# Kernel optimization log

Hardware: AMD Instinct MI355X
Metric: run time of the kernel (lower is better)

The kernel has to match this reference:

```python
import jax, jax.numpy as jnp
import numpy as np
import math

B, S, D, H, HD, R, F = 2, 2048, 1024, 16, 64, 32, 4096
EPS = 1e-5

def _layernorm(x, g, b):
    mu = jnp.mean(x, axis=-1, keepdims=True)
    var = jnp.mean(jnp.square(x - mu), axis=-1, keepdims=True)
    return (x - mu) * jax.lax.rsqrt(var + EPS) * g + b

def _gelu(x):
    # faithful tanh-approximation from the module
    c = math.sqrt(2.0 / math.pi)
    return 0.5 * x * (1.0 + jnp.tanh(c * (x + 0.044715 * x ** 3)))

def setup_inputs() -> dict:
    key = jax.random.key(0)
    ks = jax.random.split(key, 8)
    s = 0.02
    return dict(
        x=jax.random.normal(ks[0], (B, S, D), jnp.float32),
        ln1_g=jnp.ones((D,), jnp.float32), ln1_b=jnp.zeros((D,), jnp.float32),
        Wq=jax.random.normal(ks[1], (H, D, HD), jnp.float32) * s,
        bq=jnp.zeros((H, HD), jnp.float32),
        Wk=jax.random.normal(ks[2], (H, D, HD), jnp.float32) * s,
        bk=jnp.zeros((H, HD), jnp.float32),
        Wvd=jax.random.normal(ks[3], (H, D, R), jnp.float32) * s,
        bvd=jnp.zeros((H, R), jnp.float32),
        Wvu=jax.random.normal(ks[4], (H, R, HD), jnp.float32) * s,
        bvu=jnp.zeros((H, HD), jnp.float32),
        ln2_g=jnp.ones((D,), jnp.float32), ln2_b=jnp.zeros((D,), jnp.float32),
        W1=jax.random.normal(ks[5], (D, F), jnp.float32) * s,
        b1=jnp.zeros((F,), jnp.float32),
        W2=jax.random.normal(ks[6], (F, D), jnp.float32) * s,
        b2=jnp.zeros((D,), jnp.float32),
    )

def reference(x, ln1_g, ln1_b, Wq, bq, Wk, bk, Wvd, bvd, Wvu, bvu,
              ln2_g, ln2_b, W1, b1, W2, b2):
    Bx, Sx, Dx = x.shape
    y = x
    h = _layernorm(x, ln1_g, ln1_b)
    # all heads batched: [B,H,S,HD]
    q = jnp.einsum('bsd,hde->bhse', h, Wq) + bq[None, :, None, :]
    k = jnp.einsum('bsd,hde->bhse', h, Wk) + bk[None, :, None, :]
    vd = jnp.einsum('bsd,hdr->bhsr', h, Wvd) + bvd[None, :, None, :]
    v = jnp.einsum('bhsr,hre->bhse', vd, Wvu) + bvu[None, :, None, :]
    scores = jnp.einsum('bhse,bhte->bhst', q, k) / math.sqrt(Dx)  # NB: scaled by embed dim, as in source
    i = jnp.arange(Sx)
    mask = i[None, :] < i[:, None]  # key index < query index is masked (reversed causal, faithful)
    scores = jnp.where(mask[None, None, :, :], -jnp.inf, scores)
    attn = jax.nn.softmax(scores, axis=-1)
    o = jnp.einsum('bhst,bhte->bhse', attn, v)
    o = o.transpose(0, 2, 1, 3).reshape(Bx, Sx, Dx)  # concat heads
    x = o + y
    y = x
    h = _layernorm(x, ln2_g, ln2_b)
    h = _gelu(h @ W1 + b1)
    h = h @ W2 + b2
    return h + y
```

## Files before the change

kernel.cpp:

```cpp
#include <hip/hip_runtime.h>


typedef unsigned short u16;
typedef __attribute__((ext_vector_type(4))) float f32x4;
typedef __attribute__((ext_vector_type(8))) __bf16 bf16x8;

#define B_ 2
#define S_ 2048
#define D_ 1024
#define H_ 16
#define HD_ 64
#define R_ 32
#define F_ 4096
#define M_ (B_ * S_)
#define NQKV 2560
#define C2F 0.04508422002778011f

__device__ __forceinline__ u16 f2bf(float f) {
  union { float f; unsigned u; } v; v.f = f;
  unsigned u = v.u;
  return (u16)((u + 0x7FFFu + ((u >> 16) & 1u)) >> 16);
}
__device__ __forceinline__ float bf2f(u16 h) {
  union { unsigned u; float f; } v; v.u = ((unsigned)h) << 16;
  return v.f;
}
__device__ __forceinline__ unsigned pk_bf16(float lo, float hi) {
  unsigned r;
  asm volatile("v_cvt_pk_bf16_f32 %0, %1, %2" : "=v"(r) : "v"(lo), "v"(hi));
  return r;
}

typedef __attribute__((address_space(1))) void gvoid;
typedef __attribute__((address_space(3))) void lvoid;
__device__ __forceinline__ void gload_lds16(const void* g, void* l) {
  __builtin_amdgcn_global_load_lds((gvoid*)(void*)g, (lvoid*)l, 16, 0, 0);
}

__device__ __forceinline__ float gelu_f(float x) {
  float t = tanhf(0.7978845608028654f * (x + 0.044715f * x * x * x));
  return 0.5f * x * (1.0f + t);
}

__global__ __launch_bounds__(256) void wtrans(const float* __restrict__ in,
                                              u16* __restrict__ out,
                                              int Rr, int Cc, long ibs, long obs,
                                              float scale) {
  __shared__ float tile[32][33];
  const float* ip = in + (size_t)blockIdx.z * ibs;
  u16* op = out + (size_t)blockIdx.z * obs;
  int c0 = blockIdx.x * 32, r0 = blockIdx.y * 32;
  int tx = threadIdx.x & 31, ty = threadIdx.x >> 5;
#pragma unroll
  for (int j = 0; j < 32; j += 8)
    tile[ty + j][tx] = ip[(size_t)(r0 + ty + j) * Cc + c0 + tx];
  __syncthreads();
#pragma unroll
  for (int j = 0; j < 32; j += 8)
    op[(size_t)(c0 + ty + j) * Rr + r0 + tx] = f2bf(tile[tx][ty + j] * scale);
}

__global__ __launch_bounds__(256) void wconv(const float* __restrict__ in,
                                             u16* __restrict__ out, int n) {
  int i = (blockIdx.x * 256 + threadIdx.x) * 4;
  if (i < n) {
    float4 v = *(const float4*)&in[i];
    ushort4 o;
    o.x = f2bf(v.x); o.y = f2bf(v.y); o.z = f2bf(v.z); o.w = f2bf(v.w);
    *(ushort4*)&out[i] = o;
  }
}

__global__ __launch_bounds__(256) void bconcat(const float* __restrict__ bq,
                                               const float* __restrict__ bk,
                                               const float* __restrict__ bvd,
                                               float* __restrict__ o) {
  int i = blockIdx.x * 256 + threadIdx.x;
  if (i < NQKV) {
    float v = (i < 1024) ? bq[i] * C2F : (i < 2048 ? bk[i - 1024] : bvd[i - 2048]);
    o[i] = v;
  }
}

__global__ __launch_bounds__(256) void ln_kernel(const float* __restrict__ xin,
                                                 const float* __restrict__ addin,
                                                 const float* __restrict__ gam,
                                                 const float* __restrict__ bet,
                                                 u16* __restrict__ hout,
                                                 float* __restrict__ x2out) {
  int row = blockIdx.x, tid = threadIdx.x;
  size_t base = (size_t)row * D_ + tid * 4;
  float4 v = *(const float4*)&xin[base];
  if (addin) {
    float4 a = *(const float4*)&addin[base];
    v.x += a.x; v.y += a.y; v.z += a.z; v.w += a.w;
  }
  if (x2out) *(float4*)&x2out[base] = v;
  float s = v.x + v.y + v.z + v.w;
  float ss = v.x * v.x + v.y * v.y + v.z * v.z + v.w * v.w;
#pragma unroll
  for (int off = 32; off > 0; off >>= 1) {
    s += __shfl_down(s, off);
    ss += __shfl_down(ss, off);
  }
  __shared__ float red[8];
  int wv = tid >> 6;
  if ((tid & 63) == 0) { red[wv] = s; red[4 + wv] = ss; }
  __syncthreads();
  if (tid == 0) {
    float s1 = red[0] + red[1] + red[2] + red[3];
    float s2 = red[4] + red[5] + red[6] + red[7];
    float mu = s1 * (1.0f / D_);
    red[0] = mu;
    red[1] = s2 * (1.0f / D_) - mu * mu;
  }
  __syncthreads();
  float mu = red[0];
  float rstd = rsqrtf(red[1] + 1e-5f);
  int ci = tid * 4;
  ushort4 o;
  o.x = f2bf((v.x - mu) * rstd * gam[ci + 0] + bet[ci + 0]);
  o.y = f2bf((v.y - mu) * rstd * gam[ci + 1] + bet[ci + 1]);
  o.z = f2bf((v.z - mu) * rstd * gam[ci + 2] + bet[ci + 2]);
  o.w = f2bf((v.w - mu) * rstd * gam[ci + 3] + bet[ci + 3]);
  *(ushort4*)&hout[base] = o;
}

template <int MODE>
__global__ __launch_bounds__(256) void gemm_nt(const u16* __restrict__ A,
                                               const u16* __restrict__ Bt,
                                               int K, int lda, int ldb,
                                               const float* __restrict__ bias,
                                               const float* __restrict__ res,
                                               void* __restrict__ Cout,
                                               void* __restrict__ Cout2, int ldc) {
  __shared__ __align__(16) u16 As0[128 * 32];
  __shared__ __align__(16) u16 Bs0[128 * 32];
  __shared__ __align__(16) u16 As1[128 * 32];
  __shared__ __align__(16) u16 Bs1[128 * 32];
  int tid = threadIdx.x;
  int lane = tid & 63, wid = tid >> 6;
  int wm = wid >> 1, wn = wid & 1;
  int row0 = blockIdx.y * 128, col0 = blockIdx.x * 128;
  int l15 = lane & 15, g = lane >> 4;
  int srow = lane >> 2, scol = (lane & 3) * 8;
  f32x4 acc[4][4] = {};
  const u16* Ap = A + (size_t)row0 * lda;
  const u16* Bp = Bt + (size_t)col0 * ldb;

  auto STAGE = [&](u16* AS, u16* BS, int kk) {
#pragma unroll
    for (int i = 0; i < 2; ++i) {
      int c = wid * 2 + i;
      gload_lds16(Ap + (size_t)(c * 16 + srow) * lda + kk + scol, &AS[c * 512]);
      gload_lds16(Bp + (size_t)(c * 16 + srow) * ldb + kk + scol, &BS[c * 512]);
    }
  };
  auto COMPUTE = [&](const u16* AS, const u16* BS) {
    bf16x8 af[4], bfr[4];
#pragma unroll
    for (int t = 0; t < 4; ++t) {
      af[t] = *(const bf16x8*)&AS[(wm * 64 + t * 16 + l15) * 32 + g * 8];
      bfr[t] = *(const bf16x8*)&BS[(wn * 64 + t * 16 + l15) * 32 + g * 8];
    }
#pragma unroll
    for (int mt = 0; mt < 4; ++mt)
#pragma unroll
      for (int nt = 0; nt < 4; ++nt)
        acc[mt][nt] = __builtin_amdgcn_mfma_f32_16x16x32_bf16(af[mt], bfr[nt],
                                                              acc[mt][nt], 0, 0, 0);
  };

  STAGE(As0, Bs0, 0);
  __syncthreads();
  for (int k0 = 0; k0 < K; k0 += 64) {
    if (k0 + 32 < K) STAGE(As1, Bs1, k0 + 32);
    COMPUTE(As0, Bs0);
    __syncthreads();
    if (k0 + 64 < K) STAGE(As0, Bs0, k0 + 64);
    COMPUTE(As1, Bs1);
    __syncthreads();
  }

#pragma unroll
  for (int mt = 0; mt < 4; ++mt) {
#pragma unroll
    for (int nt = 0; nt < 4; ++nt) {
      int cc = col0 + wn * 64 + nt * 16 + l15;
      float bv = bias ? bias[cc] : 0.0f;
#pragma unroll
      for (int j = 0; j < 4; ++j) {
        int rr = row0 + wm * 64 + mt * 16 + g * 4 + j;
        float v = acc[mt][nt][j] + bv;
        if (MODE == 1) v = gelu_f(v);
        if (MODE == 2) {
          ((float*)Cout)[(size_t)rr * ldc + cc] = v + res[(size_t)rr * ldc + cc];
        } else {
          ((u16*)Cout)[(size_t)rr * ldc + cc] = f2bf(v);
        }
      }
    }
  }
  (void)Cout2;
}

template <int MODE>
__global__ __launch_bounds__(512, 2) void gemm8(
    const u16* __restrict__ A, const u16* __restrict__ Bt,
    int lda, int ldb, int nk,
    const float* __restrict__ bias,
    float* __restrict__ Cf, u16* __restrict__ Cb,
    u16* __restrict__ P1, u16* __restrict__ P2, u16* __restrict__ P3,
    int ldc) {
  extern __shared__ __align__(16) char smem[];
  int tid = threadIdx.x;
  int lane = tid & 63, wid = tid >> 6;
  int wm = wid >> 2, wn = wid & 3;
  int l15 = lane & 15, g = lane >> 4;
  int row0 = blockIdx.y * 256, col0 = blockIdx.x * 256;
  int koff = blockIdx.z * (nk * 64);
  const u16* Ap = A + (size_t)row0 * lda + koff;
  const u16* Bp = Bt + (size_t)col0 * ldb + koff;
  int trow = tid >> 3;
  int sbyte = ((tid & 7) * 16) ^ ((trow & 7) << 4);
  int xr = (l15 & 7) << 4;

  f32x4 acc[8][4] = {};

  auto STAGE_A = [&](int buf, int kt) {
#pragma unroll
    for (int l = 0; l < 4; ++l)
      gload_lds16((const char*)(Ap + (size_t)(l * 64 + trow) * lda + kt) + sbyte,
                  smem + buf * 65536 + (l * 64 + wid * 8) * 128);
  };
  auto STAGE_B = [&](int buf, int kt) {
#pragma unroll
    for (int l = 0; l < 4; ++l)
      gload_lds16((const char*)(Bp + (size_t)(l * 64 + trow) * ldb + kt) + sbyte,
                  smem + buf * 65536 + 32768 + (l * 64 + wid * 8) * 128);
  };

  STAGE_A(0, 0);
  STAGE_B(0, 0);
  asm volatile("s_waitcnt vmcnt(0)" ::: "memory");
  __builtin_amdgcn_sched_barrier(0);
  __builtin_amdgcn_s_barrier();

  int cur = 0;
  for (int it = 0; it < nk; ++it) {
    const char* Ab = smem + cur * 65536 + (wm * 128 + l15) * 128;
    const char* Bb = smem + cur * 65536 + 32768 + (wn * 64 + l15) * 128;
    bool nxt = (it + 1 < nk);
#pragma unroll
    for (int kk = 0; kk < 2; ++kk) {
      int kq = (kk * 64 + g * 16) ^ xr;
      bf16x8 bfr[4], af[8];
#pragma unroll
      for (int nt = 0; nt < 4; ++nt)
        bfr[nt] = *(const bf16x8*)(Bb + nt * 2048 + kq);
#pragma unroll
      for (int mt = 0; mt < 8; ++mt)
        af[mt] = *(const bf16x8*)(Ab + mt * 2048 + kq);
      if (nxt) {
        if (kk == 0) STAGE_A(cur ^ 1, (it + 1) * 64);
        else         STAGE_B(cur ^ 1, (it + 1) * 64);
      }
      __builtin_amdgcn_s_setprio(1);
#pragma unroll
      for (int mt = 0; mt < 8; ++mt)
#pragma unroll
        for (int nt = 0; nt < 4; ++nt)
          acc[mt][nt] = __builtin_amdgcn_mfma_f32_16x16x32_bf16(af[mt], bfr[nt],
                                                                acc[mt][nt], 0, 0, 0);
      __builtin_amdgcn_s_setprio(0);
    }
    asm volatile("s_waitcnt vmcnt(0)" ::: "memory");
    __builtin_amdgcn_sched_barrier(0);
    __builtin_amdgcn_s_barrier();
    cur ^= 1;
  }

  u16* pp = (u16*)nullptr;
  if (MODE == 4 && blockIdx.z != 0)
    pp = (blockIdx.z == 1) ? P1 : (blockIdx.z == 2 ? P2 : P3);
#pragma unroll
  for (int mt = 0; mt < 8; ++mt) {
#pragma unroll
    for (int nt = 0; nt < 4; ++nt) {
      int cc = col0 + wn * 64 + nt * 16 + l15;
      float bv = (MODE == 1) ? bias[cc] : 0.0f;
#pragma unroll
      for (int j = 0; j < 4; ++j) {
        int rr = row0 + wm * 128 + mt * 16 + g * 4 + j;
        float v = acc[mt][nt][j] + bv;
        if (MODE == 1) {
          Cb[(size_t)rr * ldc + cc] = f2bf(gelu_f(v));
        } else {
          if (blockIdx.z == 0) Cf[(size_t)rr * ldc + cc] = v;
          else                 pp[(size_t)rr * ldc + cc] = f2bf(v);
        }
      }
    }
  }
}

__global__ __launch_bounds__(256) void reduce2(float* __restrict__ out,
                                               const u16* __restrict__ p1,
                                               const u16* __restrict__ p2,
                                               const u16* __restrict__ p3,
                                               const float* __restrict__ b2,
                                               const float* __restrict__ x2) {
  int i = (blockIdx.x * 256 + threadIdx.x) * 4;
  float4 o = *(float4*)&out[i];
  ushort4 a = *(const ushort4*)&p1[i];
  ushort4 b = *(const ushort4*)&p2[i];
  ushort4 c = *(const ushort4*)&p3[i];
  float4 r = *(const float4*)&x2[i];
  int cix = i & (D_ - 1);
  o.x += bf2f(a.x) + bf2f(b.x) + bf2f(c.x) + b2[cix + 0] + r.x;
  o.y += bf2f(a.y) + bf2f(b.y) + bf2f(c.y) + b2[cix + 1] + r.y;
  o.z += bf2f(a.z) + bf2f(b.z) + bf2f(c.z) + b2[cix + 2] + r.z;
  o.w += bf2f(a.w) + bf2f(b.w) + bf2f(c.w) + b2[cix + 3] + r.w;
  *(float4*)&out[i] = o;
}

__global__ __launch_bounds__(256) void vu_kernel(const u16* __restrict__ vd,
                                                 const u16* __restrict__ wvu,
                                                 const float* __restrict__ bvu,
                                                 u16* __restrict__ v_t) {
  int t0 = blockIdx.x * 64, h = blockIdx.y, b = blockIdx.z;
  __shared__ u16 vds[64][32];
  __shared__ u16 vt[64][65];
  int tid = threadIdx.x;
  {
    int rr2 = tid >> 2, c8 = (tid & 3) * 8;
    *(bf16x8*)&vds[rr2][c8] =
        *(const bf16x8*)&vd[(size_t)(b * S_ + t0 + rr2) * NQKV + 2048 + h * R_ + c8];
  }
  __syncthreads();
  int e = tid & 63, tg = (tid >> 6) * 16;
  float wcol[32];
#pragma unroll
  for (int r = 0; r < 32; ++r) wcol[r] = bf2f(wvu[((size_t)h * R_ + r) * HD_ + e]);
  float bb = bvu[h * HD_ + e];
  for (int i = 0; i < 16; ++i) {
    int t = tg + i;
    float acc = bb;
#pragma unroll
    for (int r = 0; r < 32; ++r) acc += bf2f(vds[t][r]) * wcol[r];
    vt[t][e] = f2bf(acc);
  }
  __syncthreads();
  for (int idx = tid; idx < 64 * 64; idx += 256) {
    int e2 = idx >> 6, t2 = idx & 63;
    v_t[((size_t)(b * H_ + h) * HD_ + e2) * S_ + t0 + t2] = vt[t2][e2];
  }
}

__global__ __launch_bounds__(512, 2) void attn_kernel(const u16* __restrict__ cqkv,
                                                      const u16* __restrict__ v_t,
                                                      float* __restrict__ o) {
  extern __shared__ __align__(16) u16 kv[];
  __shared__ u16 Pl[8][16 * 64];
  int tid = threadIdx.x;
  int lane = tid & 63, w = tid >> 6;
  int h = blockIdx.x, b = blockIdx.y;
  int bx = blockIdx.z;
  int r = lane & 15, g = lane >> 4;
  const u16* qp = cqkv + (size_t)(b * S_) * NQKV + h * HD_;
  const u16* kp = cqkv + (size_t)(b * S_) * NQKV + 1024 + h * HD_;
  const u16* vp = v_t + (size_t)(b * H_ + h) * HD_ * S_;
  u16* Pw = Pl[w];

  int srow = w * 8 + (lane >> 3);
  int ssw = ((lane & 7) * 16) ^ (((lane >> 3) & 7) << 4);

  int xr = (r & 7) << 4;
  int kq0 = ((g * 16) ^ xr) >> 1;
  int kq1 = ((64 + g * 16) ^ xr) >> 1;

  auto STAGE = [&](int buf, int kt) {
    u16* base = kv + buf * 8192;
    gload_lds16((const char*)(kp + (size_t)(kt + srow) * NQKV) + ssw,
                base + w * 512);
    gload_lds16((const char*)(vp + (size_t)srow * S_ + kt) + ssw,
                base + 4096 + w * 512);
  };

#pragma unroll 1
  for (int half = 0; half < 2; ++half) {
    int qb = half ? (S_ - 128) - bx * 128 : bx * 128;
    int s0 = qb + w * 16;
    int qrow = s0 + r;

    gload_lds16((const char*)(qp + (size_t)(s0 + (lane >> 3)) * NQKV) + ssw, Pw);
    gload_lds16((const char*)(qp + (size_t)(s0 + 8 + (lane >> 3)) * NQKV) + ssw,
                Pw + 512);
    asm volatile("s_waitcnt vmcnt(0)" ::: "memory");
    __builtin_amdgcn_sched_barrier(0);
    __builtin_amdgcn_s_barrier();
    __builtin_amdgcn_sched_barrier(0);
    bf16x8 aq0 = *(const bf16x8*)&Pw[(r << 6) + kq0];
    bf16x8 aq1 = *(const bf16x8*)&Pw[(r << 6) + kq1];

    f32x4 oa[4] = {};
    float m_ = -1e30f, l_ = 0.0f;

    int nt = (S_ - qb) >> 6;
    STAGE(0, qb);
    STAGE(1, qb + 64);

    for (int it = 0; it < nt; ++it) {
      int kt = qb + it * 64;
      if (it + 1 < nt) {
        asm volatile("s_waitcnt vmcnt(2)" ::: "memory");
      } else {
        asm volatile("s_waitcnt vmcnt(0)" ::: "memory");
      }
      __builtin_amdgcn_sched_barrier(0);
      __builtin_amdgcn_s_barrier();
      __builtin_amdgcn_sched_barrier(0);
      if (it + 2 < nt) STAGE((it + 2) % 3, qb + (it + 2) * 64);

      if (kt + 64 > s0) {
        const u16* Kb = kv + (it % 3) * 8192;
        const u16* Vb = Kb + 4096;

        f32x4 sc[4] = {};
#pragma unroll
        for (int blk = 0; blk < 4; ++blk) {
          bf16x8 a0 = *(const bf16x8*)&Kb[((blk * 16 + r) << 6) + kq0];
          bf16x8 a1 = *(const bf16x8*)&Kb[((blk * 16 + r) << 6) + kq1];
          sc[blk] = __builtin_amdgcn_mfma_f32_16x16x32_bf16(a0, aq0, sc[blk], 0, 0, 0);
          sc[blk] = __builtin_amdgcn_mfma_f32_16x16x32_bf16(a1, aq1, sc[blk], 0, 0, 0);
        }

        float p[16];
        if ((qrow & ~63) == kt) {
#pragma unroll
          for (int blk = 0; blk < 4; ++blk)
#pragma unroll
            for (int j = 0; j < 4; ++j) {
              int kk = kt + blk * 16 + g * 4 + j;
              p[blk * 4 + j] = (kk < qrow) ? -1e30f : sc[blk][j];
            }
        } else {
#pragma unroll
          for (int blk = 0; blk < 4; ++blk)
#pragma unroll
            for (int j = 0; j < 4; ++j) p[blk * 4 + j] = sc[blk][j];
        }
        float mx = p[0];
#pragma unroll
        for (int i = 1; i < 16; ++i) mx = fmaxf(mx, p[i]);
        mx = fmaxf(mx, __shfl_xor(mx, 16));
        mx = fmaxf(mx, __shfl_xor(mx, 32));
        float mn = fmaxf(m_, mx);
        float scl = __builtin_amdgcn_exp2f(m_ - mn);
        m_ = mn;
        float sm = 0.0f;
#pragma unroll
        for (int i = 0; i < 16; ++i) {
          p[i] = __builtin_amdgcn_exp2f(p[i] - mn);
          sm += p[i];
        }
        sm += __shfl_xor(sm, 16);
        sm += __shfl_xor(sm, 32);
        l_ = l_ * scl + sm;
#pragma unroll
        for (int et = 0; et < 4; ++et) oa[et] *= scl;

#pragma unroll
        for (int blk = 0; blk < 4; ++blk) {
          uint2 pk;
          pk.x = pk_bf16(p[blk * 4 + 0], p[blk * 4 + 1]);
          pk.y = pk_bf16(p[blk * 4 + 2], p[blk * 4 + 3]);
          *(uint2*)&Pw[(r << 6) + ((((blk << 5) + (g << 3)) ^ xr) >> 1)] = pk;
        }
        asm volatile("s_waitcnt lgkmcnt(0)" ::: "memory");
        __builtin_amdgcn_sched_barrier(0);
        bf16x8 pb0 = *(const bf16x8*)&Pw[(r << 6) + kq0];
        bf16x8 pb1 = *(const bf16x8*)&Pw[(r << 6) + kq1];
#pragma unroll
        for (int et = 0; et < 4; ++et) {
          bf16x8 v0 = *(const bf16x8*)&Vb[((et * 16 + r) << 6) + kq0];
          bf16x8 v1 = *(const bf16x8*)&Vb[((et * 16 + r) << 6) + kq1];
          oa[et] = __builtin_amdgcn_mfma_f32_16x16x32_bf16(v0, pb0, oa[et], 0, 0, 0);
          oa[et] = __builtin_amdgcn_mfma_f32_16x16x32_bf16(v1, pb1, oa[et], 0, 0, 0);
        }
      }
    }

    float inv = 1.0f / l_;
#pragma unroll
    for (int et = 0; et < 4; ++et)
#pragma unroll
      for (int j = 0; j < 4; ++j)
        o[(size_t)(b * S_ + s0 + r) * D_ + h * HD_ + et * 16 + g * 4 + j] =
            oa[et][j] * inv;
  }
}

namespace {
struct GemmAttrInit {
  GemmAttrInit() {
    hipFuncSetAttribute((const void*)gemm8<1>,
                        hipFuncAttributeMaxDynamicSharedMemorySize, 131072);
    hipFuncSetAttribute((const void*)gemm8<4>,
                        hipFuncAttributeMaxDynamicSharedMemorySize, 131072);
    hipFuncSetAttribute((const void*)attn_kernel,
                        hipFuncAttributeMaxDynamicSharedMemorySize, 49152);
  }
};
GemmAttrInit _gemm_attr_init;
}

extern "C" void kernel_launch(void* const* d_in, const int* in_sizes, int n_in,
                              void* d_out, int out_size, void* d_ws, size_t ws_size,
                              hipStream_t stream) {
  const float* x = (const float*)d_in[0];
  const float* ln1_g = (const float*)d_in[1];
  const float* ln1_b = (const float*)d_in[2];
  const float* Wq = (const float*)d_in[3];
  const float* bq = (const float*)d_in[4];
  const float* Wk = (const float*)d_in[5];
  const float* bk = (const float*)d_in[6];
  const float* Wvd = (const float*)d_in[7];
  const float* bvd = (const float*)d_in[8];
  const float* Wvu = (const float*)d_in[9];
  const float* bvu = (const float*)d_in[10];
  const float* ln2_g = (const float*)d_in[11];
  const float* ln2_b = (const float*)d_in[12];
  const float* W1 = (const float*)d_in[13];
  const float* b1 = (const float*)d_in[14];
  const float* W2 = (const float*)d_in[15];
  const float* b2 = (const float*)d_in[16];
  float* out = (float*)d_out;
  (void)in_sizes; (void)n_in; (void)out_size; (void)ws_size;

  char* ws = (char*)d_ws;
  const size_t MB = 1024 * 1024;
  const size_t KB = 1024;
  u16* wqkvT = (u16*)(ws + 0);
  u16* wvuB = (u16*)(ws + 5 * MB);
  float* bqkv = (float*)(ws + 5 * MB + 64 * KB);
  u16* w1T = (u16*)(ws + 5 * MB + 384 * KB);
  u16* w2T = (u16*)(ws + 13 * MB + 384 * KB);
  u16* hbuf = (u16*)(ws + 21 * MB + 384 * KB);
  u16* cqkv = (u16*)(ws + 29 * MB + 384 * KB);
  u16* vT = (u16*)(ws + 49 * MB + 384 * KB);
  float* ob = (float*)(ws + 57 * MB + 384 * KB);
  float* x2 = (float*)(ws + 73 * MB + 384 * KB);
  u16* ubuf = cqkv;
  u16* p1 = (u16*)(ws + 0);
  u16* p2 = (u16*)hbuf;
  u16* p3 = (u16*)vT;

  dim3 blk(256);
  wtrans<<<dim3(2, 32, 16), blk, 0, stream>>>(Wq, wqkvT, 1024, 64, 65536L, 65536L, C2F);
  wtrans<<<dim3(2, 32, 16), blk, 0, stream>>>(Wk, wqkvT + 1024 * 1024, 1024, 64,
                                              65536L, 65536L, 1.0f);
  wtrans<<<dim3(1, 32, 16), blk, 0, stream>>>(Wvd, wqkvT + 2048 * 1024, 1024, 32,
                                              32768L, 32768L, 1.0f);
  wconv<<<dim3(32), blk, 0, stream>>>(Wvu, wvuB, H_ * R_ * HD_);
  bconcat<<<dim3(10), blk, 0, stream>>>(bq, bk, bvd, bqkv);
  wtrans<<<dim3(128, 32, 1), blk, 0, stream>>>(W1, w1T, 1024, 4096, 0L, 0L, 1.0f);
  wtrans<<<dim3(32, 128, 1), blk, 0, stream>>>(W2, w2T, 4096, 1024, 0L, 0L, 1.0f);
  ln_kernel<<<dim3(M_), blk, 0, stream>>>(x, (const float*)nullptr, ln1_g, ln1_b,
                                          hbuf, (float*)nullptr);
  gemm_nt<0><<<dim3(20, 32), blk, 0, stream>>>(hbuf, wqkvT, 1024, 1024, 1024, bqkv,
                                               (const float*)nullptr, (void*)cqkv,
                                               (void*)nullptr, NQKV);
  vu_kernel<<<dim3(S_ / 64, H_, B_), blk, 0, stream>>>(cqkv, wvuB, bvu, vT);
  attn_kernel<<<dim3(H_, B_, 8), dim3(512), 49152, stream>>>(cqkv, vT, ob);
  ln_kernel<<<dim3(M_), blk, 0, stream>>>(x, ob, ln2_g, ln2_b, hbuf, x2);
  gemm8<1><<<dim3(16, 16, 1), dim3(512), 131072, stream>>>(
      hbuf, w1T, 1024, 1024, 16, b1, (float*)nullptr, ubuf,
      (u16*)nullptr, (u16*)nullptr, (u16*)nullptr, 4096);
  gemm8<4><<<dim3(4, 16, 4), dim3(512), 131072, stream>>>(
      ubuf, w2T, 4096, 4096, 16, (const float*)nullptr, out, (u16*)nullptr,
      p1, p2, p3, 1024);
  reduce2<<<dim3(M_ * D_ / 1024), blk, 0, stream>>>(out, p1, p2, p3, b2, x2);
}
```

Before: 232.4 us.

## Switch FFN GEMM to triple-buffered K=32 tiles with prefetch two ahead

Restructures the 256x256 FFN GEMM main loop from a double-buffered K=64 tile, with A and B staged in separate halves, to a three-stage ring of K=32 tiles. Loads run two iterations ahead and each step waits with a partial vmcnt. Dynamic LDS drops from 128KB to 96KB and the XOR swizzle is removed. This aims to hide global-load latency better and let more blocks fit per CU, but it doubles the number of barriers per K step and risks LDS bank conflicts without the swizzle.

```diff
diff --git a/kernel.cpp b/kernel.cpp
--- a/kernel.cpp
+++ b/kernel.cpp
@@ -218,66 +218,56 @@
   int wm = wid >> 2, wn = wid & 3;
   int l15 = lane & 15, g = lane >> 4;
   int row0 = blockIdx.y * 256, col0 = blockIdx.x * 256;
-  int koff = blockIdx.z * (nk * 64);
+  int koff = (MODE == 4) ? blockIdx.z * (nk * 32) : 0;
   const u16* Ap = A + (size_t)row0 * lda + koff;
   const u16* Bp = Bt + (size_t)col0 * ldb + koff;
-  int trow = tid >> 3;
-  int sbyte = ((tid & 7) * 16) ^ ((trow & 7) << 4);
-  int xr = (l15 & 7) << 4;
+  int srow = tid >> 2;
+  int scol = (tid & 3) * 8;
 
   f32x4 acc[8][4] = {};
 
-  auto STAGE_A = [&](int buf, int kt) {
-#pragma unroll
-    for (int l = 0; l < 4; ++l)
-      gload_lds16((const char*)(Ap + (size_t)(l * 64 + trow) * lda + kt) + sbyte,
-                  smem + buf * 65536 + (l * 64 + wid * 8) * 128);
+  auto STAGE = [&](int buf, int kt) {
+#pragma unroll
+    for (int i = 0; i < 2; ++i)
+      gload_lds16(Ap + (size_t)(i * 128 + srow) * lda + kt + scol,
+                  smem + buf * 32768 + i * 8192 + wid * 1024);
+#pragma unroll
+    for (int i = 0; i < 2; ++i)
+      gload_lds16(Bp + (size_t)(i * 128 + srow) * ldb + kt + scol,
+                  smem + buf * 32768 + 16384 + i * 8192 + wid * 1024);
   };
-  auto STAGE_B = [&](int buf, int kt) {
-#pragma unroll
-    for (int l = 0; l < 4; ++l)
-      gload_lds16((const char*)(Bp + (size_t)(l * 64 + trow) * ldb + kt) + sbyte,
-                  smem + buf * 65536 + 32768 + (l * 64 + wid * 8) * 128);
-  };
-
-  STAGE_A(0, 0);
-  STAGE_B(0, 0);
-  asm volatile("s_waitcnt vmcnt(0)" ::: "memory");
-  __builtin_amdgcn_sched_barrier(0);
-  __builtin_amdgcn_s_barrier();
-
-  int cur = 0;
+
+  STAGE(0, 0);
+  STAGE(1, 32);
+
   for (int it = 0; it < nk; ++it) {
-    const char* Ab = smem + cur * 65536 + (wm * 128 + l15) * 128;
-    const char* Bb = smem + cur * 65536 + 32768 + (wn * 64 + l15) * 128;
-    bool nxt = (it + 1 < nk);
-#pragma unroll
-    for (int kk = 0; kk < 2; ++kk) {
-      int kq = (kk * 64 + g * 16) ^ xr;
-      bf16x8 bfr[4], af[8];
-#pragma unroll
-      for (int nt = 0; nt < 4; ++nt)
-        bfr[nt] = *(const bf16x8*)(Bb + nt * 2048 + kq);
-#pragma unroll
-      for (int mt = 0; mt < 8; ++mt)
-        af[mt] = *(const bf16x8*)(Ab + mt * 2048 + kq);
-      if (nxt) {
-        if (kk == 0) STAGE_A(cur ^ 1, (it + 1) * 64);
-        else         STAGE_B(cur ^ 1, (it + 1) * 64);
-      }
-      __builtin_amdgcn_s_setprio(1);
-#pragma unroll
-      for (int mt = 0; mt < 8; ++mt)
-#pragma unroll
-        for (int nt = 0; nt < 4; ++nt)
-          acc[mt][nt] = __builtin_amdgcn_mfma_f32_16x16x32_bf16(af[mt], bfr[nt],
-                                                                acc[mt][nt], 0, 0, 0);
-      __builtin_amdgcn_s_setprio(0);
+    if (it + 1 < nk) {
+      asm volatile("s_waitcnt vmcnt(4)" ::: "memory");
+    } else {
+      asm volatile("s_waitcnt vmcnt(0)" ::: "memory");
     }
-    asm volatile("s_waitcnt vmcnt(0)" ::: "memory");
     __builtin_amdgcn_sched_barrier(0);
     __builtin_amdgcn_s_barrier();
-    cur ^= 1;
+    __builtin_amdgcn_sched_barrier(0);
+    if (it + 2 < nk) STAGE((it + 2) % 3, (it + 2) * 32);
+
+    const char* Ab = smem + (it % 3) * 32768 + (size_t)(wm * 128 + l15) * 64;
+    const char* Bb = smem + (it % 3) * 32768 + 16384 + (size_t)(wn * 64 + l15) * 64;
+    bf16x8 af[8], bfr[4];
+#pragma unroll
+    for (int nt = 0; nt < 4; ++nt)
+      bfr[nt] = *(const bf16x8*)(Bb + nt * 1024 + g * 16);
+#pragma unroll
+    for (int mt = 0; mt < 8; ++mt)
+      af[mt] = *(const bf16x8*)(Ab + mt * 1024 + g * 16);
+    __builtin_amdgcn_s_setprio(1);
+#pragma unroll
+    for (int mt = 0; mt < 8; ++mt)
+#pragma unroll
+      for (int nt = 0; nt < 4; ++nt)
+        acc[mt][nt] = __builtin_amdgcn_mfma_f32_16x16x32_bf16(af[mt], bfr[nt],
+                                                              acc[mt][nt], 0, 0, 0);
+    __builtin_amdgcn_s_setprio(0);
   }
 
   u16* pp = (u16*)nullptr;
@@ -505,9 +495,9 @@
 struct GemmAttrInit {
   GemmAttrInit() {
     hipFuncSetAttribute((const void*)gemm8<1>,
-                        hipFuncAttributeMaxDynamicSharedMemorySize, 131072);
+                        hipFuncAttributeMaxDynamicSharedMemorySize, 98304);
     hipFuncSetAttribute((const void*)gemm8<4>,
-                        hipFuncAttributeMaxDynamicSharedMemorySize, 131072);
+                        hipFuncAttributeMaxDynamicSharedMemorySize, 98304);
     hipFuncSetAttribute((const void*)attn_kernel,
                         hipFuncAttributeMaxDynamicSharedMemorySize, 49152);
   }
@@ -574,11 +564,11 @@
   vu_kernel<<<dim3(S_ / 64, H_, B_), blk, 0, stream>>>(cqkv, wvuB, bvu, vT);
   attn_kernel<<<dim3(H_, B_, 8), dim3(512), 49152, stream>>>(cqkv, vT, ob);
   ln_kernel<<<dim3(M_), blk, 0, stream>>>(x, ob, ln2_g, ln2_b, hbuf, x2);
-  gemm8<1><<<dim3(16, 16, 1), dim3(512), 131072, stream>>>(
-      hbuf, w1T, 1024, 1024, 16, b1, (float*)nullptr, ubuf,
+  gemm8<1><<<dim3(16, 16, 1), dim3(512), 98304, stream>>>(
+      hbuf, w1T, 1024, 1024, 32, b1, (float*)nullptr, ubuf,
       (u16*)nullptr, (u16*)nullptr, (u16*)nullptr, 4096);
-  gemm8<4><<<dim3(4, 16, 4), dim3(512), 131072, stream>>>(
-      ubuf, w2T, 4096, 4096, 16, (const float*)nullptr, out, (u16*)nullptr,
+  gemm8<4><<<dim3(4, 16, 4), dim3(512), 98304, stream>>>(
+      ubuf, w2T, 4096, 4096, 32, (const float*)nullptr, out, (u16*)nullptr,
       p1, p2, p3, 1024);
   reduce2<<<dim3(M_ * D_ / 1024), blk, 0, stream>>>(out, p1, p2, p3, b2, x2);
 }
```

Measured after the change: 236.1 us. Within noise of the previous version (+1.6%).
